# Kernel optimization log

Measured on AMD Instinct MI355X. Metric: run time of the kernel, lower is better.

## Reference

```python
import jax, jax.numpy as jnp
import numpy as np

B, S, E, H, DK = 16, 512, 256, 8, 32
NSH, NSEL = 2, 4           # shared heads, selected dynamic heads
NDYN = H - NSH             # dynamic heads
NB = 4                     # num_blocks -> blocks_1: NB layers, blocks_2: 2*NB layers
L = 3 * NB                 # total layers, params stacked on leading dim
NSKILL, NQ = 1000, 10000
FC1, FC2 = 512, 256


def setup_inputs():
    key = jax.random.key(0)
    ks = jax.random.split(key, 24)
    r = lambda i, sh: jax.random.normal(ks[i], sh, jnp.float32) * 0.02
    return {
        'skills': jax.random.randint(ks[0], (B, S), 0, NSKILL),
        'responses': jax.random.randint(ks[1], (B, S), 0, 2),
        'questions': jax.random.randint(ks[2], (B, S), 0, NQ),
        'attention_mask': jnp.ones((B, S), jnp.int32),
        'q_embed': r(3, (NSKILL, E)),
        'qa_embed': r(4, (3, E)),
        'q_embed_diff': r(5, (NSKILL + 1, E)),
        'qa_embed_diff': r(6, (2 * NSKILL + 1, E)),
        'difficult_param': r(7, (NQ + 1, 1)),
        'Wq': r(8, (L, E, E)), 'bq': jnp.zeros((L, E)),
        'Wv': r(9, (L, E, E)), 'bv': jnp.zeros((L, E)),
        'Wo': r(10, (L, E, E)), 'bo': jnp.zeros((L, E)),
        'Wg': r(11, (L, E, NDYN)),
        'ln1_g': jnp.ones((L, E)), 'ln1_b': jnp.zeros((L, E)),
        'ln2_g': jnp.ones((L, E)), 'ln2_b': jnp.zeros((L, E)),
        'ffn_W1': r(12, (L, E, E)), 'ffn_b1': jnp.zeros((L, E)),
        'ffn_W2': r(13, (L, E, E)), 'ffn_b2': jnp.zeros((L, E)),
        'out_W1': r(14, (2 * E, FC1)), 'out_b1': jnp.zeros((FC1,)),
        'out_W2': r(15, (FC1, FC2)), 'out_b2': jnp.zeros((FC2,)),
        'out_W3': r(16, (FC2, 1)), 'out_b3': jnp.zeros((1,)),
    }


def _ln(x, g, b):
    m = x.mean(-1, keepdims=True)
    v = ((x - m) ** 2).mean(-1, keepdims=True)
    return (x - m) * jax.lax.rsqrt(v + 1e-5) * g + b


def _layer(i, q_in, k_in, v_in, mask, P):
    # MoH attention: standard MHA + top-k routed dynamic heads (kq_same=True)
    qh = (q_in @ P['Wq'][i] + P['bq'][i]).reshape(B, S, H, DK).transpose(0, 2, 1, 3)
    kh = (k_in @ P['Wq'][i] + P['bq'][i]).reshape(B, S, H, DK).transpose(0, 2, 1, 3)
    vh = (v_in @ P['Wv'][i] + P['bv'][i]).reshape(B, S, H, DK).transpose(0, 2, 1, 3)
    scores = jnp.einsum('bhid,bhjd->bhij', qh, kh) / np.float32(np.sqrt(DK))
    attn = jax.nn.softmax(jnp.where(mask, scores, -1e32), axis=-1)
    ctx = jnp.einsum('bhij,bhjd->bhid', attn, vh).transpose(0, 2, 1, 3)  # [B,S,H,DK]
    # router on pre-projection query: hard top-NSEL one-hot gates over NDYN heads
    logits = q_in @ P['Wg'][i]                     # [B,S,NDYN]
    _, topi = jax.lax.top_k(logits, NSEL)
    gates = jax.nn.one_hot(topi, NDYN, dtype=ctx.dtype).sum(-2)
    hg = jnp.concatenate([jnp.ones((B, S, NSH), ctx.dtype), gates], axis=-1)  # [B,S,H]
    attn_out = (ctx * hg[..., None]).reshape(B, S, E) @ P['Wo'][i] + P['bo'][i]
    x = _ln(q_in + attn_out, P['ln1_g'][i], P['ln1_b'][i])
    f = jax.nn.relu(x @ P['ffn_W1'][i] + P['ffn_b1'][i]) @ P['ffn_W2'][i] + P['ffn_b2'][i]
    return _ln(x + f, P['ln2_g'][i], P['ln2_b'][i])


def _forward(skills, responses, questions, P):
    masked_r = responses * (responses > -1).astype(responses.dtype)
    q_emb = P['q_embed'][skills]
    qa_emb = q_emb + P['qa_embed'][masked_r]
    q_diff = P['q_embed_diff'][skills]
    pid = P['difficult_param'][questions]          # [B,S,1]
    q_emb = q_emb + pid * q_diff
    qa_diff = P['qa_embed_diff'][skills + NSKILL * masked_r]
    qa_emb = qa_emb + pid * (qa_diff + q_diff)
    idx = jnp.arange(S)
    causal = (idx[None, :] <= idx[:, None])[None, None]  # mask==1: incl diagonal
    strict = (idx[None, :] < idx[:, None])[None, None]   # mask==0: excl diagonal
    y, x = qa_emb, q_emb
    for i in range(NB):
        y = _layer(i, y, y, y, causal, P)
    li = NB
    for _ in range(NB):
        x = _layer(li, x, x, x, causal, P); li += 1
        x = _layer(li, x, x, y, strict, P); li += 1
    h = jnp.concatenate([x, q_emb], axis=-1)
    h = jax.nn.relu(h @ P['out_W1'] + P['out_b1'])
    h = jax.nn.relu(h @ P['out_W2'] + P['out_b2'])
    out = jax.nn.sigmoid(h @ P['out_W3'] + P['out_b3'])[..., 0]
    return out[:, 1:]


def reference(skills, responses, questions, attention_mask, q_embed, qa_embed, q_embed_diff, qa_embed_diff, difficult_param, Wq, bq, Wv, bv, Wo, bo, Wg, ln1_g, ln1_b, ln2_g, ln2_b, ffn_W1, ffn_b1, ffn_W2, ffn_b2, out_W1, out_b1, out_W2, out_b2, out_W3, out_b3):
    P = dict(q_embed=q_embed, qa_embed=qa_embed, q_embed_diff=q_embed_diff, qa_embed_diff=qa_embed_diff, difficult_param=difficult_param, Wq=Wq, bq=bq, Wv=Wv, bv=bv, Wo=Wo, bo=bo, Wg=Wg, ln1_g=ln1_g, ln1_b=ln1_b, ln2_g=ln2_g, ln2_b=ln2_b, ffn_W1=ffn_W1, ffn_b1=ffn_b1, ffn_W2=ffn_W2, ffn_b2=ffn_b2, out_W1=out_W1, out_b1=out_b1, out_W2=out_W2, out_b2=out_b2, out_W3=out_W3, out_b3=out_b3)
    return _forward(skills, responses, questions, P)
```

## Files before the change

### kernel.cpp

```cpp
#include <hip/hip_runtime.h>
#include <hip/hip_bf16.h>
#include <type_traits>

constexpr int CB = 16, CS = 512, CE = 256, CH = 8, CDK = 32;
constexpr int CNDYN = 6;
constexpr int CT = CB * CS;
constexpr float SCALE = 0.17677669529663687f;

typedef __bf16 bf16x8 __attribute__((ext_vector_type(8)));
typedef float f32x4 __attribute__((ext_vector_type(4)));
typedef unsigned short u16x8 __attribute__((ext_vector_type(8)));

__device__ __forceinline__ unsigned short f2bf(float x) {
    union { float f; unsigned u; } v; v.f = x;
    unsigned r = v.u + 0x7fff + ((v.u >> 16) & 1);
    return (unsigned short)(r >> 16);
}

__global__ __launch_bounds__(256) void embed_kernel(
    const int* __restrict__ skills, const int* __restrict__ responses,
    const int* __restrict__ questions,
    const float* __restrict__ q_embed, const float* __restrict__ qa_embed,
    const float* __restrict__ q_embed_diff, const float* __restrict__ qa_embed_diff,
    const float* __restrict__ difficult,
    float* __restrict__ q_emb, float* __restrict__ qa_emb, float* __restrict__ xb)
{
    int t = blockIdx.x;
    int e = threadIdx.x;
    int sk = skills[t];
    int r  = responses[t];
    r = (r > -1) ? r : 0;
    float pid = difficult[questions[t]];
    float qe  = q_embed[(size_t)sk * CE + e];
    float qd  = q_embed_diff[(size_t)sk * CE + e];
    float qv  = qe + pid * qd;
    float qae = qe + qa_embed[(size_t)r * CE + e];
    float qad = qa_embed_diff[((size_t)sk + 1000 * r) * CE + e];
    float qav = qae + pid * (qad + qd);
    q_emb[(size_t)t * CE + e]  = qv;
    xb[(size_t)t * CE + e]     = qv;
    qa_emb[(size_t)t * CE + e] = qav;
}

__device__ __forceinline__ void transpose_tile(
    const float* __restrict__ src, unsigned short* __restrict__ dst, int K, int N)
{
    __shared__ unsigned short T[64][72];
    int k0 = blockIdx.y * 64, n0 = blockIdx.x * 64;
    int t = threadIdx.x;
    int kr = t >> 3, nsg = (t & 7) * 8;
#pragma unroll
    for (int rr = 0; rr < 64; rr += 32) {
        const float* p = src + (size_t)(k0 + kr + rr) * N + n0 + nsg;
        float4 a = *reinterpret_cast<const float4*>(p);
        float4 b = *reinterpret_cast<const float4*>(p + 4);
        int k = kr + rr;
        T[nsg + 0][k] = f2bf(a.x); T[nsg + 1][k] = f2bf(a.y);
        T[nsg + 2][k] = f2bf(a.z); T[nsg + 3][k] = f2bf(a.w);
        T[nsg + 4][k] = f2bf(b.x); T[nsg + 5][k] = f2bf(b.y);
        T[nsg + 6][k] = f2bf(b.z); T[nsg + 7][k] = f2bf(b.w);
    }
    __syncthreads();
    {
        int n = t >> 2, ks = (t & 3) * 16;
        unsigned short* dp = dst + (size_t)(n0 + n) * K + k0 + ks;
        *reinterpret_cast<u16x8*>(dp)     = *reinterpret_cast<const u16x8*>(&T[n][ks]);
        *reinterpret_cast<u16x8*>(dp + 8) = *reinterpret_cast<const u16x8*>(&T[n][ks + 8]);
    }
}

__global__ __launch_bounds__(256) void prep_w_layers(
    const float* __restrict__ Wq, const float* __restrict__ Wv,
    const float* __restrict__ Wo, const float* __restrict__ W1,
    const float* __restrict__ W2,
    unsigned short* __restrict__ qvT, unsigned short* __restrict__ woT,
    unsigned short* __restrict__ w1T, unsigned short* __restrict__ w2T)
{
    int z = blockIdx.z;
    int which = z / 12, l = z % 12;
    const float* src;
    unsigned short* dst;
    if      (which == 0) { src = Wq + (size_t)l * 65536; dst = qvT + (size_t)l * 131072; }
    else if (which == 1) { src = Wv + (size_t)l * 65536; dst = qvT + (size_t)l * 131072 + 65536; }
    else if (which == 2) { src = Wo + (size_t)l * 65536; dst = woT + (size_t)l * 65536; }
    else if (which == 3) { src = W1 + (size_t)l * 65536; dst = w1T + (size_t)l * 65536; }
    else                 { src = W2 + (size_t)l * 65536; dst = w2T + (size_t)l * 65536; }
    transpose_tile(src, dst, 256, 256);
}

__global__ __launch_bounds__(256) void prep_w_one(
    const float* __restrict__ src, unsigned short* __restrict__ dst, int K, int N)
{
    transpose_tile(src, dst, K, N);
}

template <typename TA, typename TC>
__global__ __launch_bounds__(256) void gemm_mfma(
    const TA* __restrict__ A, const unsigned short* __restrict__ WT,
    const float* __restrict__ bias, TC* __restrict__ C,
    const float* __restrict__ bias2, TC* __restrict__ C2,
    int M, int N, int K, int relu, int split)
{
    __shared__ __attribute__((aligned(16))) unsigned short As[64][72];
    __shared__ __attribute__((aligned(16))) unsigned short Bs[64][72];
    int tid = threadIdx.x;
    int bm = blockIdx.y * 64, bn = blockIdx.x * 64;
    int w = tid >> 6, lane = tid & 63;
    int wr = w >> 1, wc = w & 1;
    int lo = lane & 15, hi = lane >> 4;
    int srow = tid >> 2, sseg = (tid & 3) * 16;
    f32x4 acc[2][2] = {};

    for (int kk = 0; kk < K; kk += 64) {
        if constexpr (std::is_same<TA, float>::value) {
            const float* ap = A + (size_t)(bm + srow) * K + kk + sseg;
            float4 a0 = *reinterpret_cast<const float4*>(ap);
            float4 a1 = *reinterpret_cast<const float4*>(ap + 4);
            float4 a2 = *reinterpret_cast<const float4*>(ap + 8);
            float4 a3 = *reinterpret_cast<const float4*>(ap + 12);
            u16x8 p0, p1;
            p0[0]=f2bf(a0.x); p0[1]=f2bf(a0.y); p0[2]=f2bf(a0.z); p0[3]=f2bf(a0.w);
            p0[4]=f2bf(a1.x); p0[5]=f2bf(a1.y); p0[6]=f2bf(a1.z); p0[7]=f2bf(a1.w);
            p1[0]=f2bf(a2.x); p1[1]=f2bf(a2.y); p1[2]=f2bf(a2.z); p1[3]=f2bf(a2.w);
            p1[4]=f2bf(a3.x); p1[5]=f2bf(a3.y); p1[6]=f2bf(a3.z); p1[7]=f2bf(a3.w);
            *reinterpret_cast<u16x8*>(&As[srow][sseg])     = p0;
            *reinterpret_cast<u16x8*>(&As[srow][sseg + 8]) = p1;
        } else {
            const unsigned short* ap = A + (size_t)(bm + srow) * K + kk + sseg;
            *reinterpret_cast<u16x8*>(&As[srow][sseg])     = *reinterpret_cast<const u16x8*>(ap);
            *reinterpret_cast<u16x8*>(&As[srow][sseg + 8]) = *reinterpret_cast<const u16x8*>(ap + 8);
        }
        {
            const unsigned short* bp = WT + (size_t)(bn + srow) * K + kk + sseg;
            *reinterpret_cast<u16x8*>(&Bs[srow][sseg])     = *reinterpret_cast<const u16x8*>(bp);
            *reinterpret_cast<u16x8*>(&Bs[srow][sseg + 8]) = *reinterpret_cast<const u16x8*>(bp + 8);
        }
        __syncthreads();
#pragma unroll
        for (int ks = 0; ks < 2; ++ks) {
            bf16x8 a0 = *reinterpret_cast<const bf16x8*>(&As[wr * 32 + lo][ks * 32 + hi * 8]);
            bf16x8 a1 = *reinterpret_cast<const bf16x8*>(&As[wr * 32 + 16 + lo][ks * 32 + hi * 8]);
            bf16x8 b0 = *reinterpret_cast<const bf16x8*>(&Bs[wc * 32 + lo][ks * 32 + hi * 8]);
            bf16x8 b1 = *reinterpret_cast<const bf16x8*>(&Bs[wc * 32 + 16 + lo][ks * 32 + hi * 8]);
            acc[0][0] = __builtin_amdgcn_mfma_f32_16x16x32_bf16(a0, b0, acc[0][0], 0, 0, 0);
            acc[0][1] = __builtin_amdgcn_mfma_f32_16x16x32_bf16(a0, b1, acc[0][1], 0, 0, 0);
            acc[1][0] = __builtin_amdgcn_mfma_f32_16x16x32_bf16(a1, b0, acc[1][0], 0, 0, 0);
            acc[1][1] = __builtin_amdgcn_mfma_f32_16x16x32_bf16(a1, b1, acc[1][1], 0, 0, 0);
        }
        __syncthreads();
    }
    const float* bp = bias;
    TC* Cp = C;
    int ldc = split ? split : N;
    int cb = bn;
    if (split && bn >= split) { bp = bias2; Cp = C2; ldc = N - split; cb = bn - split; }
#pragma unroll
    for (int i = 0; i < 2; ++i)
#pragma unroll
        for (int j = 0; j < 2; ++j) {
            int col = cb + wc * 32 + j * 16 + lo;
            float bv = bp[col];
#pragma unroll
            for (int r = 0; r < 4; ++r) {
                int row = bm + wr * 32 + i * 16 + hi * 4 + r;
                float v = acc[i][j][r] + bv;
                if (relu) v = fmaxf(v, 0.f);
                if constexpr (std::is_same<TC, float>::value)
                    Cp[(size_t)row * ldc + col] = v;
                else
                    Cp[(size_t)row * ldc + col] = f2bf(v);
            }
        }
}

__global__ __launch_bounds__(512) void attn_mfma(
    const unsigned short* __restrict__ Q, const unsigned short* __restrict__ V,
    unsigned short* __restrict__ Ctx, const unsigned char* __restrict__ gm,
    int strict)
{
    __shared__ __attribute__((aligned(16))) unsigned short Ks[512][40];
    __shared__ __attribute__((aligned(16))) unsigned short VTc[8][32][72];
    __shared__ __attribute__((aligned(16))) unsigned short Ps[8][16][72];

    int blk = blockIdx.x;
    int half = blk & 1;
    int h = (blk >> 1) & 7;
    int b = blk >> 4;
    int tid = threadIdx.x;
    int w = tid >> 6, lane = tid & 63;
    int lo = lane & 15, hi = lane >> 4;

#pragma unroll
    for (int r = 0; r < 4; ++r) {
        int row = (tid >> 2) + r * 128;
        int d0 = (tid & 3) * 8;
        u16x8 kv = *reinterpret_cast<const u16x8*>(Q + ((size_t)b * CS + row) * CE + h * 32 + d0);
        *reinterpret_cast<u16x8*>(&Ks[row][d0]) = kv;
        u16x8 vv = *reinterpret_cast<const u16x8*>(V + ((size_t)b * CS + row) * CE + h * 32 + d0);
        int c8 = row >> 6, kc = row & 63;
        VTc[c8][d0+0][kc]=vv[0]; VTc[c8][d0+1][kc]=vv[1];
        VTc[c8][d0+2][kc]=vv[2]; VTc[c8][d0+3][kc]=vv[3];
        VTc[c8][d0+4][kc]=vv[4]; VTc[c8][d0+5][kc]=vv[5];
        VTc[c8][d0+6][kc]=vv[6]; VTc[c8][d0+7][kc]=vv[7];
    }
    __syncthreads();

    for (int it = 0; it < 2; ++it) {
        int gg = half * 16 + w + it * 8;
        int qg0 = gg * 16;
        int qg = qg0 + lo;
        bool uni = strict && (qg == 0);
        bf16x8 qfrag = *reinterpret_cast<const bf16x8*>(&Ks[qg0 + lo][hi * 8]);

        f32x4 ctx0 = {0.f,0.f,0.f,0.f}, ctx1 = {0.f,0.f,0.f,0.f};
        float m = -1e30f, l = 0.f;
        int nch = (strict && qg0 == 0) ? 8 : ((gg >> 2) + 1);

        for (int c = 0; c < nch; ++c) {
            f32x4 sacc[4];
#pragma unroll
            for (int kt = 0; kt < 4; ++kt) {
                bf16x8 kfrag = *reinterpret_cast<const bf16x8*>(&Ks[c * 64 + kt * 16 + lo][hi * 8]);
                f32x4 z = {0.f,0.f,0.f,0.f};
                sacc[kt] = __builtin_amdgcn_mfma_f32_16x16x32_bf16(kfrag, qfrag, z, 0, 0, 0);
            }
            float sv[16];
            float mt = -1e30f;
#pragma unroll
            for (int kt = 0; kt < 4; ++kt)
#pragma unroll
                for (int r = 0; r < 4; ++r) {
                    int kidx = c * 64 + kt * 16 + hi * 4 + r;
                    float s = sacc[kt][r] * SCALE;
                    bool valid = strict ? (kidx < qg) : (kidx <= qg);
                    s = valid ? s : -1e30f;
                    if (uni) s = 0.f;
                    sv[kt * 4 + r] = s;
                    mt = fmaxf(mt, s);
                }
            mt = fmaxf(mt, __shfl_xor(mt, 16));
            mt = fmaxf(mt, __shfl_xor(mt, 32));
            float mn = fmaxf(m, mt);
            float co = __expf(m - mn);
            float lt = 0.f;
#pragma unroll
            for (int i = 0; i < 16; ++i) {
                float p = __expf(sv[i] - mn);
                sv[i] = p;
                lt += p;
            }
            lt += __shfl_xor(lt, 16);
            lt += __shfl_xor(lt, 32);
            l = l * co + lt;
            m = mn;
#pragma unroll
            for (int r = 0; r < 4; ++r) { ctx0[r] *= co; ctx1[r] *= co; }
#pragma unroll
            for (int kt = 0; kt < 4; ++kt) {
                unsigned short* pd = &Ps[w][lo][kt * 16 + hi * 4];
                pd[0] = f2bf(sv[kt * 4 + 0]); pd[1] = f2bf(sv[kt * 4 + 1]);
                pd[2] = f2bf(sv[kt * 4 + 2]); pd[3] = f2bf(sv[kt * 4 + 3]);
            }
            asm volatile("s_waitcnt lgkmcnt(0)" ::: "memory");
            __builtin_amdgcn_sched_barrier(0);
#pragma unroll
            for (int kh = 0; kh < 2; ++kh) {
                bf16x8 pfrag = *reinterpret_cast<const bf16x8*>(&Ps[w][lo][kh * 32 + hi * 8]);
                bf16x8 v0 = *reinterpret_cast<const bf16x8*>(&VTc[c][lo][kh * 32 + hi * 8]);
                bf16x8 v1 = *reinterpret_cast<const bf16x8*>(&VTc[c][16 + lo][kh * 32 + hi * 8]);
                ctx0 = __builtin_amdgcn_mfma_f32_16x16x32_bf16(v0, pfrag, ctx0, 0, 0, 0);
                ctx1 = __builtin_amdgcn_mfma_f32_16x16x32_bf16(v1, pfrag, ctx1, 0, 0, 0);
            }
        }

        float inv = 1.f / l;
        float* cb = reinterpret_cast<float*>(&Ps[w][0][0]);
#pragma unroll
        for (int r = 0; r < 4; ++r) {
            cb[lo * 36 + (hi * 4 + r)]      = ctx0[r] * inv;
            cb[lo * 36 + (16 + hi * 4 + r)] = ctx1[r] * inv;
        }
        asm volatile("s_waitcnt lgkmcnt(0)" ::: "memory");
        __builtin_amdgcn_sched_barrier(0);
        {
            int qloc = lane >> 2, d0 = (lane & 3) * 8;
            const float* src = cb + qloc * 36 + d0;
            int i = qg0 + qloc;
            float mf = ((gm[(size_t)b * CS + i] >> h) & 1) ? 1.f : 0.f;
            u16x8 o;
#pragma unroll
            for (int k = 0; k < 8; ++k) o[k] = f2bf(src[k] * mf);
            *reinterpret_cast<u16x8*>(Ctx + ((size_t)b * CS + i) * CE + h * 32 + d0) = o;
        }
        asm volatile("s_waitcnt lgkmcnt(0)" ::: "memory");
        __builtin_amdgcn_sched_barrier(0);
    }
}

__global__ __launch_bounds__(512) void gate_mask(
    const float* __restrict__ qin, const float* __restrict__ Wg,
    unsigned char* __restrict__ mb)
{
    int w = threadIdx.x >> 6, lane = threadIdx.x & 63;
    int t = blockIdx.x * 8 + w;
    const float* q = qin + (size_t)t * CE;
    float p[CNDYN] = {};
#pragma unroll
    for (int r = 0; r < 4; ++r) {
        int e = lane + r * 64;
        float qe = q[e];
        const float* wg = &Wg[(size_t)e * CNDYN];
#pragma unroll
        for (int j = 0; j < CNDYN; ++j) p[j] += qe * wg[j];
    }
#pragma unroll
    for (int o = 32; o > 0; o >>= 1)
#pragma unroll
        for (int j = 0; j < CNDYN; ++j) p[j] += __shfl_down(p[j], o);
    if (lane == 0) {
        int mask = 3;
        for (int j = 0; j < CNDYN; ++j) {
            int rank = 0;
            for (int k = 0; k < CNDYN; ++k)
                if (p[k] > p[j] || (p[k] == p[j] && k < j)) rank++;
            if (rank < 4) mask |= 1 << (2 + j);
        }
        mb[t] = (unsigned char)mask;
    }
}

__global__ __launch_bounds__(256) void add_ln(
    const float* __restrict__ A, const float* __restrict__ Bv,
    const float* __restrict__ g, const float* __restrict__ bb,
    float* __restrict__ O)
{
    int w = threadIdx.x >> 6, lane = threadIdx.x & 63;
    int t = blockIdx.x * 4 + w;
    size_t base = (size_t)t * CE + lane * 4;
    float4 a = *reinterpret_cast<const float4*>(A + base);
    float4 b = *reinterpret_cast<const float4*>(Bv + base);
    float4 v = {a.x + b.x, a.y + b.y, a.z + b.z, a.w + b.w};
    float s = v.x + v.y + v.z + v.w;
#pragma unroll
    for (int o = 32; o > 0; o >>= 1) s += __shfl_xor(s, o);
    float mean = s * (1.f / CE);
    float4 d = {v.x - mean, v.y - mean, v.z - mean, v.w - mean};
    float s2 = d.x * d.x + d.y * d.y + d.z * d.z + d.w * d.w;
#pragma unroll
    for (int o = 32; o > 0; o >>= 1) s2 += __shfl_xor(s2, o);
    float rstd = rsqrtf(s2 * (1.f / CE) + 1e-5f);
    float4 gg = *reinterpret_cast<const float4*>(g + lane * 4);
    float4 bv4 = *reinterpret_cast<const float4*>(bb + lane * 4);
    float4 o4 = {d.x * rstd * gg.x + bv4.x, d.y * rstd * gg.y + bv4.y,
                 d.z * rstd * gg.z + bv4.z, d.w * rstd * gg.w + bv4.w};
    *reinterpret_cast<float4*>(O + base) = o4;
}

__global__ __launch_bounds__(256) void concat_kernel(
    const float* __restrict__ x, const float* __restrict__ qe,
    unsigned short* __restrict__ cat)
{
    int t = blockIdx.x, e = threadIdx.x;
    int o = e * 2;
    float2 v;
    if (o < 256) v = *reinterpret_cast<const float2*>(&x[(size_t)t * CE + o]);
    else         v = *reinterpret_cast<const float2*>(&qe[(size_t)t * CE + o - 256]);
    unsigned pk = (unsigned)f2bf(v.x) | ((unsigned)f2bf(v.y) << 16);
    *reinterpret_cast<unsigned*>(&cat[(size_t)t * 512 + o]) = pk;
}

__global__ __launch_bounds__(64) void final_kernel(
    const float* __restrict__ H2, const float* __restrict__ W3,
    const float* __restrict__ b3, float* __restrict__ out)
{
    int t = blockIdx.x, lane = threadIdx.x;
    const float* h = H2 + (size_t)t * CE;
    float s = 0.f;
#pragma unroll
    for (int r = 0; r < 4; ++r) {
        int e = lane + r * 64;
        s += h[e] * W3[e];
    }
#pragma unroll
    for (int o = 32; o > 0; o >>= 1) s += __shfl_down(s, o);
    if (lane == 0) {
        float v = 1.f / (1.f + __expf(-(s + b3[0])));
        int b = t >> 9, si = t & 511;
        if (si > 0) out[(size_t)b * (CS - 1) + si - 1] = v;
    }
}

extern "C" void kernel_launch(void* const* d_in, const int* in_sizes, int n_in,
                              void* d_out, int out_size, void* d_ws, size_t ws_size,
                              hipStream_t stream)
{
    const int* skills    = (const int*)d_in[0];
    const int* responses = (const int*)d_in[1];
    const int* questions = (const int*)d_in[2];
    const float* q_embed       = (const float*)d_in[4];
    const float* qa_embed      = (const float*)d_in[5];
    const float* q_embed_diff  = (const float*)d_in[6];
    const float* qa_embed_diff = (const float*)d_in[7];
    const float* difficult     = (const float*)d_in[8];
    const float* Wq = (const float*)d_in[9];  const float* bq = (const float*)d_in[10];
    const float* Wv = (const float*)d_in[11]; const float* bv = (const float*)d_in[12];
    const float* Wo = (const float*)d_in[13]; const float* bo = (const float*)d_in[14];
    const float* Wg = (const float*)d_in[15];
    const float* ln1g = (const float*)d_in[16]; const float* ln1b = (const float*)d_in[17];
    const float* ln2g = (const float*)d_in[18]; const float* ln2b = (const float*)d_in[19];
    const float* fW1 = (const float*)d_in[20]; const float* fb1 = (const float*)d_in[21];
    const float* fW2 = (const float*)d_in[22]; const float* fb2 = (const float*)d_in[23];
    const float* oW1 = (const float*)d_in[24]; const float* ob1 = (const float*)d_in[25];
    const float* oW2 = (const float*)d_in[26]; const float* ob2 = (const float*)d_in[27];
    const float* oW3 = (const float*)d_in[28]; const float* ob3 = (const float*)d_in[29];
    float* out = (float*)d_out;

    char* ws = (char*)d_ws;
    const size_t R = (size_t)CT * CE * sizeof(float);
    float* q_emb = (float*)(ws + 0 * R);
    float* xb    = (float*)(ws + 1 * R);
    float* yb    = (float*)(ws + 2 * R);
    float* S0f   = (float*)(ws + 3 * R);
    float* S1f   = (float*)(ws + 4 * R);
    float* S2f   = (float*)(ws + 5 * R);
    unsigned short* S0b = (unsigned short*)S0f;
    unsigned short* S1b = (unsigned short*)S1f;
    unsigned short* S2b = (unsigned short*)S2f;
    unsigned short* qvT = (unsigned short*)(ws + 7 * R);
    unsigned short* woT = qvT + (size_t)12 * 131072;
    unsigned short* w1T = woT + (size_t)12 * 65536;
    unsigned short* w2T = w1T + (size_t)12 * 65536;
    unsigned short* o1T = w2T + (size_t)12 * 65536;
    unsigned short* o2T = o1T + (size_t)512 * 512;
    unsigned char* maskbuf = (unsigned char*)(o2T + (size_t)256 * 512);
    (void)in_sizes; (void)n_in; (void)out_size; (void)ws_size;

    prep_w_layers<<<dim3(4, 4, 60), 256, 0, stream>>>(Wq, Wv, Wo, fW1, fW2, qvT, woT, w1T, w2T);
    prep_w_one<<<dim3(8, 8), 256, 0, stream>>>(oW1, o1T, 512, 512);
    prep_w_one<<<dim3(4, 8), 256, 0, stream>>>(oW2, o2T, 512, 256);

    embed_kernel<<<CT, 256, 0, stream>>>(skills, responses, questions,
        q_embed, qa_embed, q_embed_diff, qa_embed_diff, difficult, q_emb, yb, xb);

    auto layer = [&](int li, const float* qin, const float* vin, float* outc, int strict) {
        if (qin == vin) {
            gemm_mfma<float, unsigned short><<<dim3(8, 128), 256, 0, stream>>>(
                qin, qvT + (size_t)li * 131072, bq + (size_t)li * CE, S0b,
                bv + (size_t)li * CE, S1b, CT, 512, CE, 0, 256);
        } else {
            gemm_mfma<float, unsigned short><<<dim3(4, 128), 256, 0, stream>>>(
                qin, qvT + (size_t)li * 131072, bq + (size_t)li * CE, S0b,
                nullptr, nullptr, CT, CE, CE, 0, 0);
            gemm_mfma<float, unsigned short><<<dim3(4, 128), 256, 0, stream>>>(
                vin, qvT + (size_t)li * 131072 + 65536, bv + (size_t)li * CE, S1b,
                nullptr, nullptr, CT, CE, CE, 0, 0);
        }
        gate_mask<<<CT / 8, 512, 0, stream>>>(qin, Wg + (size_t)li * CE * CNDYN, maskbuf);
        attn_mfma<<<CB * CH * 2, 512, 0, stream>>>(S0b, S1b, S2b, maskbuf, strict);
        gemm_mfma<unsigned short, float><<<dim3(4, 128), 256, 0, stream>>>(
            S2b, woT + (size_t)li * 65536, bo + (size_t)li * CE, S0f,
            nullptr, nullptr, CT, CE, CE, 0, 0);
        add_ln<<<CT / 4, 256, 0, stream>>>(qin, S0f, ln1g + (size_t)li * CE, ln1b + (size_t)li * CE, S1f);
        gemm_mfma<float, unsigned short><<<dim3(4, 128), 256, 0, stream>>>(
            S1f, w1T + (size_t)li * 65536, fb1 + (size_t)li * CE, S2b,
            nullptr, nullptr, CT, CE, CE, 1, 0);
        gemm_mfma<unsigned short, float><<<dim3(4, 128), 256, 0, stream>>>(
            S2b, w2T + (size_t)li * 65536, fb2 + (size_t)li * CE, S0f,
            nullptr, nullptr, CT, CE, CE, 0, 0);
        add_ln<<<CT / 4, 256, 0, stream>>>(S1f, S0f, ln2g + (size_t)li * CE, ln2b + (size_t)li * CE, outc);
    };

    for (int i = 0; i < 4; ++i) layer(i, yb, yb, yb, 0);
    int li = 4;
    for (int r = 0; r < 4; ++r) {
        layer(li, xb, xb, xb, 0); li++;
        layer(li, xb, yb, xb, 1); li++;
    }

    concat_kernel<<<CT, 256, 0, stream>>>(xb, q_emb, S0b);
    gemm_mfma<unsigned short, unsigned short><<<dim3(8, 128), 256, 0, stream>>>(
        S0b, o1T, ob1, S2b, nullptr, nullptr, CT, 512, 512, 1, 0);
    gemm_mfma<unsigned short, float><<<dim3(4, 128), 256, 0, stream>>>(
        S2b, o2T, ob2, xb, nullptr, nullptr, CT, 256, 512, 1, 0);
    final_kernel<<<CT, 64, 0, stream>>>(xb, oW3, ob3, out);
}
```

Before: 1.183 ms.

## Fuse out-projection, residual LayerNorm and FFN GEMMs into full-row tail kernels

Replaces the post-attention sequence of out-proj GEMM, add+LN, FFN1 GEMM, FFN2 GEMM and add+LN with two kernels that each own 32 full rows. The first does Wo GEMM plus bias, residual add and LayerNorm, writes x1 in fp32, then runs FFN1 with ReLU from shared memory. The second does FFN2 plus residual and LayerNorm. This removes several launches and the intermediate fp32 round trips. In exchange, each block reloads the full 256x256 weight per row-tile, and the large shared-memory footprint limits occupancy.

```diff
diff --git a/kernel.cpp b/kernel.cpp
--- a/kernel.cpp
+++ b/kernel.cpp
@@ -173,6 +173,160 @@
         }
 }
 
+template <int DO_FFN>
+__global__ __launch_bounds__(512) void fused_tail(
+    const unsigned short* __restrict__ Abf, const unsigned short* __restrict__ WT1,
+    const float* __restrict__ bias1, const float* __restrict__ res,
+    const float* __restrict__ g, const float* __restrict__ bvec,
+    float* __restrict__ xout,
+    const unsigned short* __restrict__ WT2, const float* __restrict__ bias2,
+    unsigned short* __restrict__ Hout)
+{
+    __shared__ __attribute__((aligned(16))) unsigned short A_s[32][264];
+    __shared__ __attribute__((aligned(16))) unsigned short Bs[256][72];
+    __shared__ float res_s[32][260];
+    __shared__ float bias_s[256], g_s[256], b_s[256];
+    __shared__ float red_s[256];
+
+    int tid = threadIdx.x;
+    int brow = blockIdx.x * 32;
+    int w = tid >> 6, lane = tid & 63;
+    int wr = w >> 2, wc = w & 3;
+    int lo = lane & 15, hi = lane >> 4;
+    int rowb = wr * 16 + hi * 4;
+
+    {
+        int row = tid >> 4, seg = (tid & 15) * 16;
+        const unsigned short* ap = Abf + (size_t)(brow + row) * CE + seg;
+        *reinterpret_cast<u16x8*>(&A_s[row][seg])     = *reinterpret_cast<const u16x8*>(ap);
+        *reinterpret_cast<u16x8*>(&A_s[row][seg + 8]) = *reinterpret_cast<const u16x8*>(ap + 8);
+        const float* rp = res + (size_t)(brow + row) * CE + seg;
+#pragma unroll
+        for (int q = 0; q < 4; ++q)
+            *reinterpret_cast<float4*>(&res_s[row][seg + q * 4]) = *reinterpret_cast<const float4*>(rp + q * 4);
+        if (tid < 256) { bias_s[tid] = bias1[tid]; b_s[tid] = bvec[tid]; }
+        else           { g_s[tid - 256] = g[tid - 256]; }
+    }
+
+    f32x4 acc[4] = {};
+    for (int kc = 0; kc < 4; ++kc) {
+        int k0 = kc * 64;
+        __syncthreads();
+        {
+            int n = tid >> 1, half = (tid & 1) * 32;
+            const unsigned short* bp = WT1 + (size_t)n * CE + k0 + half;
+#pragma unroll
+            for (int q = 0; q < 4; ++q)
+                *reinterpret_cast<u16x8*>(&Bs[n][half + q * 8]) = *reinterpret_cast<const u16x8*>(bp + q * 8);
+        }
+        __syncthreads();
+#pragma unroll
+        for (int sub = 0; sub < 2; ++sub) {
+            bf16x8 a = *reinterpret_cast<const bf16x8*>(&A_s[wr * 16 + lo][k0 + sub * 32 + hi * 8]);
+#pragma unroll
+            for (int nt = 0; nt < 4; ++nt) {
+                bf16x8 b = *reinterpret_cast<const bf16x8*>(&Bs[wc * 64 + nt * 16 + lo][sub * 32 + hi * 8]);
+                acc[nt] = __builtin_amdgcn_mfma_f32_16x16x32_bf16(a, b, acc[nt], 0, 0, 0);
+            }
+        }
+    }
+    __syncthreads();
+
+    float vv[4][4];
+    float part[4] = {};
+#pragma unroll
+    for (int nt = 0; nt < 4; ++nt) {
+        int col = wc * 64 + nt * 16 + lo;
+        float bc = bias_s[col];
+#pragma unroll
+        for (int rr = 0; rr < 4; ++rr) {
+            float v = acc[nt][rr] + bc + res_s[rowb + rr][col];
+            vv[nt][rr] = v; part[rr] += v;
+        }
+    }
+#pragma unroll
+    for (int rr = 0; rr < 4; ++rr)
+#pragma unroll
+        for (int m = 1; m < 16; m <<= 1) part[rr] += __shfl_xor(part[rr], m);
+    if (lo == 0) {
+#pragma unroll
+        for (int rr = 0; rr < 4; ++rr) red_s[(rowb + rr) * 4 + wc] = part[rr];
+    }
+    __syncthreads();
+    float mean[4], sq[4] = {};
+#pragma unroll
+    for (int rr = 0; rr < 4; ++rr) {
+        float4 q = *reinterpret_cast<const float4*>(&red_s[(rowb + rr) * 4]);
+        mean[rr] = (q.x + q.y + q.z + q.w) * (1.f / 256.f);
+    }
+#pragma unroll
+    for (int nt = 0; nt < 4; ++nt)
+#pragma unroll
+        for (int rr = 0; rr < 4; ++rr) { float d = vv[nt][rr] - mean[rr]; sq[rr] += d * d; }
+#pragma unroll
+    for (int rr = 0; rr < 4; ++rr)
+#pragma unroll
+        for (int m = 1; m < 16; m <<= 1) sq[rr] += __shfl_xor(sq[rr], m);
+    if (lo == 0) {
+#pragma unroll
+        for (int rr = 0; rr < 4; ++rr) red_s[128 + (rowb + rr) * 4 + wc] = sq[rr];
+    }
+    __syncthreads();
+    float rstd[4];
+#pragma unroll
+    for (int rr = 0; rr < 4; ++rr) {
+        float4 q = *reinterpret_cast<const float4*>(&red_s[128 + (rowb + rr) * 4]);
+        rstd[rr] = rsqrtf((q.x + q.y + q.z + q.w) * (1.f / 256.f) + 1e-5f);
+    }
+#pragma unroll
+    for (int nt = 0; nt < 4; ++nt) {
+        int col = wc * 64 + nt * 16 + lo;
+        float gc = g_s[col], bc = b_s[col];
+#pragma unroll
+        for (int rr = 0; rr < 4; ++rr) {
+            float x = (vv[nt][rr] - mean[rr]) * rstd[rr] * gc + bc;
+            xout[(size_t)(brow + rowb + rr) * CE + col] = x;
+            if (DO_FFN) A_s[rowb + rr][col] = f2bf(x);
+        }
+    }
+
+    if (DO_FFN) {
+        f32x4 acc2[4] = {};
+        for (int kc = 0; kc < 4; ++kc) {
+            int k0 = kc * 64;
+            __syncthreads();
+            {
+                int n = tid >> 1, half = (tid & 1) * 32;
+                const unsigned short* bp = WT2 + (size_t)n * CE + k0 + half;
+#pragma unroll
+                for (int q = 0; q < 4; ++q)
+                    *reinterpret_cast<u16x8*>(&Bs[n][half + q * 8]) = *reinterpret_cast<const u16x8*>(bp + q * 8);
+                if (kc == 0 && tid < 256) bias_s[tid] = bias2[tid];
+            }
+            __syncthreads();
+#pragma unroll
+            for (int sub = 0; sub < 2; ++sub) {
+                bf16x8 a = *reinterpret_cast<const bf16x8*>(&A_s[wr * 16 + lo][k0 + sub * 32 + hi * 8]);
+#pragma unroll
+                for (int nt = 0; nt < 4; ++nt) {
+                    bf16x8 b = *reinterpret_cast<const bf16x8*>(&Bs[wc * 64 + nt * 16 + lo][sub * 32 + hi * 8]);
+                    acc2[nt] = __builtin_amdgcn_mfma_f32_16x16x32_bf16(a, b, acc2[nt], 0, 0, 0);
+                }
+            }
+        }
+#pragma unroll
+        for (int nt = 0; nt < 4; ++nt) {
+            int col = wc * 64 + nt * 16 + lo;
+            float bc = bias_s[col];
+#pragma unroll
+            for (int rr = 0; rr < 4; ++rr) {
+                float hv = fmaxf(acc2[nt][rr] + bc, 0.f);
+                Hout[(size_t)(brow + rowb + rr) * CE + col] = f2bf(hv);
+            }
+        }
+    }
+}
+
 __global__ __launch_bounds__(512) void attn_mfma(
     const unsigned short* __restrict__ Q, const unsigned short* __restrict__ V,
     unsigned short* __restrict__ Ctx, const unsigned char* __restrict__ gm,
@@ -327,33 +481,6 @@
         }
         mb[t] = (unsigned char)mask;
     }
-}
-
-__global__ __launch_bounds__(256) void add_ln(
-    const float* __restrict__ A, const float* __restrict__ Bv,
-    const float* __restrict__ g, const float* __restrict__ bb,
-    float* __restrict__ O)
-{
-    int w = threadIdx.x >> 6, lane = threadIdx.x & 63;
-    int t = blockIdx.x * 4 + w;
-    size_t base = (size_t)t * CE + lane * 4;
-    float4 a = *reinterpret_cast<const float4*>(A + base);
-    float4 b = *reinterpret_cast<const float4*>(Bv + base);
-    float4 v = {a.x + b.x, a.y + b.y, a.z + b.z, a.w + b.w};
-    float s = v.x + v.y + v.z + v.w;
-#pragma unroll
-    for (int o = 32; o > 0; o >>= 1) s += __shfl_xor(s, o);
-    float mean = s * (1.f / CE);
-    float4 d = {v.x - mean, v.y - mean, v.z - mean, v.w - mean};
-    float s2 = d.x * d.x + d.y * d.y + d.z * d.z + d.w * d.w;
-#pragma unroll
-    for (int o = 32; o > 0; o >>= 1) s2 += __shfl_xor(s2, o);
-    float rstd = rsqrtf(s2 * (1.f / CE) + 1e-5f);
-    float4 gg = *reinterpret_cast<const float4*>(g + lane * 4);
-    float4 bv4 = *reinterpret_cast<const float4*>(bb + lane * 4);
-    float4 o4 = {d.x * rstd * gg.x + bv4.x, d.y * rstd * gg.y + bv4.y,
-                 d.z * rstd * gg.z + bv4.z, d.w * rstd * gg.w + bv4.w};
-    *reinterpret_cast<float4*>(O + base) = o4;
 }
 
 __global__ __launch_bounds__(256) void concat_kernel(
@@ -423,6 +550,7 @@
     float* S0f   = (float*)(ws + 3 * R);
     float* S1f   = (float*)(ws + 4 * R);
     float* S2f   = (float*)(ws + 5 * R);
+    float* x1buf = (float*)(ws + 6 * R);
     unsigned short* S0b = (unsigned short*)S0f;
     unsigned short* S1b = (unsigned short*)S1f;
     unsigned short* S2b = (unsigned short*)S2f;
@@ -457,17 +585,14 @@
         }
         gate_mask<<<CT / 8, 512, 0, stream>>>(qin, Wg + (size_t)li * CE * CNDYN, maskbuf);
         attn_mfma<<<CB * CH * 2, 512, 0, stream>>>(S0b, S1b, S2b, maskbuf, strict);
-        gemm_mfma<unsigned short, float><<<dim3(4, 128), 256, 0, stream>>>(
-            S2b, woT + (size_t)li * 65536, bo + (size_t)li * CE, S0f,
-            nullptr, nullptr, CT, CE, CE, 0, 0);
-        add_ln<<<CT / 4, 256, 0, stream>>>(qin, S0f, ln1g + (size_t)li * CE, ln1b + (size_t)li * CE, S1f);
-        gemm_mfma<float, unsigned short><<<dim3(4, 128), 256, 0, stream>>>(
-            S1f, w1T + (size_t)li * 65536, fb1 + (size_t)li * CE, S2b,
-            nullptr, nullptr, CT, CE, CE, 1, 0);
-        gemm_mfma<unsigned short, float><<<dim3(4, 128), 256, 0, stream>>>(
-            S2b, w2T + (size_t)li * 65536, fb2 + (size_t)li * CE, S0f,
-            nullptr, nullptr, CT, CE, CE, 0, 0);
-        add_ln<<<CT / 4, 256, 0, stream>>>(S1f, S0f, ln2g + (size_t)li * CE, ln2b + (size_t)li * CE, outc);
+        fused_tail<1><<<CT / 32, 512, 0, stream>>>(
+            S2b, woT + (size_t)li * 65536, bo + (size_t)li * CE, qin,
+            ln1g + (size_t)li * CE, ln1b + (size_t)li * CE, x1buf,
+            w1T + (size_t)li * 65536, fb1 + (size_t)li * CE, S0b);
+        fused_tail<0><<<CT / 32, 512, 0, stream>>>(
+            S0b, w2T + (size_t)li * 65536, fb2 + (size_t)li * CE, x1buf,
+            ln2g + (size_t)li * CE, ln2b + (size_t)li * CE, outc,
+            nullptr, nullptr, nullptr);
     };
 
     for (int i = 0; i < 4; ++i) layer(i, yb, yb, yb, 0);
```

Measured after the change: 1.072 ms. 1.1x faster.
